# Optimization experiments

Measured on AMD Instinct MI355X. Metric: run time of the kernel, lower is better.

Reference implementation:

```python
import jax, jax.numpy as jnp
import numpy as np

N = 50000
E = 500000
IN_F = 128
HEADS = 4
NEG_SLOPE = 0.2


def _gatv2_conv(x, src, dst, Wl, Wr, att, bias, concat):
    # PyG GATv2Conv (share_weights=False): x_l = lin_l(x) for source, x_r = lin_r(x) for target
    n = x.shape[0]
    H, C = att.shape
    xl = (x @ Wl.T).reshape(n, H, C)
    xr = (x @ Wr.T).reshape(n, H, C)
    # per-edge: e_ij = att . leaky_relu(xl[j] + xr[i])
    e = jax.nn.leaky_relu(xl[src] + xr[dst], negative_slope=NEG_SLOPE)  # [E,H,C]
    logit = jnp.einsum('ehc,hc->eh', e, att)  # [E,H]
    # segment softmax over destination node
    lmax = jax.ops.segment_max(logit, dst, num_segments=n)
    lmax = jnp.where(jnp.isfinite(lmax), lmax, 0.0)
    w = jnp.exp(logit - lmax[dst])
    denom = jax.ops.segment_sum(w, dst, num_segments=n)
    alpha = w / (denom[dst] + 1e-16)
    # weighted scatter-aggregate of source messages
    out = jax.ops.segment_sum(xl[src] * alpha[:, :, None], dst, num_segments=n)  # [N,H,C]
    if concat:
        return out.reshape(n, H * C) + bias
    return out.mean(axis=1) + bias


def setup_inputs() -> dict:
    key = jax.random.key(0)
    ks = jax.random.split(key, 11)
    s = 0.1
    x = jax.random.normal(ks[0], (N, IN_F), jnp.float32)
    edge_index = jax.random.randint(ks[1], (2, E), 0, N, dtype=jnp.int32)
    # layer 1: in=128 -> heads=4, C=32, concat -> out 128
    Wl1 = jax.random.normal(ks[2], (128, IN_F), jnp.float32) * s
    Wr1 = jax.random.normal(ks[3], (128, IN_F), jnp.float32) * s
    att1 = jax.random.normal(ks[4], (HEADS, 32), jnp.float32) * s
    b1 = jnp.zeros((128,), jnp.float32)
    # layer 2: in=128 -> heads=4, C=64, mean (concat=False) -> out 64
    Wl2 = jax.random.normal(ks[5], (256, 128), jnp.float32) * s
    Wr2 = jax.random.normal(ks[6], (256, 128), jnp.float32) * s
    att2 = jax.random.normal(ks[7], (HEADS, 64), jnp.float32) * s
    b2 = jnp.zeros((64,), jnp.float32)
    return {"x": x, "edge_index": edge_index, "Wl1": Wl1, "Wr1": Wr1, "att1": att1,
            "b1": b1, "Wl2": Wl2, "Wr2": Wr2, "att2": att2, "b2": b2}


def reference(x, edge_index, Wl1, Wr1, att1, b1, Wl2, Wr2, att2, b2):
    n = x.shape[0]
    loops = jnp.arange(n, dtype=edge_index.dtype)
    src = jnp.concatenate([edge_index[0], loops])  # PyG add_self_loops=True
    dst = jnp.concatenate([edge_index[1], loops])
    # dropout inactive (inference); forward body: elu between layers
    h = jax.nn.elu(_gatv2_conv(x, src, dst, Wl1, Wr1, att1, b1, concat=True))
    logits = _gatv2_conv(h, src, dst, Wl2, Wr2, att2, b2, concat=False)
    return logits
```

## Files before the change

### kernel.cpp

```cpp
#include <hip/hip_runtime.h>
#include <hip/hip_bf16.h>
#include <math.h>


typedef _Float16 half2v __attribute__((ext_vector_type(2)));
typedef _Float16 half4v __attribute__((ext_vector_type(4)));
typedef _Float16 half8v __attribute__((ext_vector_type(8)));
typedef float float4v __attribute__((ext_vector_type(4)));

template <int CTRL>
static __device__ __forceinline__ float dppadd(float x) {
  int y = __builtin_amdgcn_update_dpp(0, __float_as_int(x), CTRL, 0xf, 0xf, true);
  return x + __int_as_float(y);
}

static __device__ __forceinline__ float red16dpp(float p) {
  p = dppadd<0xB1>(p);
  p = dppadd<0x4E>(p);
  p = dppadd<0x140>(p);
  p = dppadd<0x141>(p);
  return p;
}


__global__ void cvt_all_kernel(const float* __restrict__ x,
                               const float* __restrict__ wl1, const float* __restrict__ wr1,
                               const float* __restrict__ wl2, const float* __restrict__ wr2,
                               _Float16* __restrict__ xb, _Float16* __restrict__ wb, int n4x) {
  int i = blockIdx.x * blockDim.x + threadIdx.x;
  int stride = gridDim.x * blockDim.x;
  int total = n4x + 24576;
  for (; i < total; i += stride) {
    if (i < n4x) {
      float4 v = ((const float4*)x)[i];
      half4v o = {(_Float16)v.x, (_Float16)v.y, (_Float16)v.z, (_Float16)v.w};
      ((half4v*)xb)[i] = o;
    } else {
      int fj = (i - n4x) * 4;
      const float* src;
      int so;
      if (fj < 16384) { src = wl1; so = fj; }
      else if (fj < 32768) { src = wr1; so = fj - 16384; }
      else if (fj < 65536) { src = wl2; so = fj - 32768; }
      else { src = wr2; so = fj - 65536; }
      float4 v = *(const float4*)(src + so);
      half4v o = {(_Float16)v.x, (_Float16)v.y, (_Float16)v.z, (_Float16)v.w};
      *(half4v*)(wb + fj) = o;
    }
  }
}


__global__ void count_kernel(const int* __restrict__ dst, int* __restrict__ deg, int E) {
  int i = blockIdx.x * blockDim.x + threadIdx.x;
  if (i < E) atomicAdd(&deg[dst[i]], 1);
}

__global__ void partial_kernel(const int* __restrict__ deg, int* __restrict__ partial, int N) {
  int t = threadIdx.x;
  int i = blockIdx.x * 256 + t;
  int v = (i < N) ? deg[i] : 0;
  v += __shfl_xor(v, 1); v += __shfl_xor(v, 2); v += __shfl_xor(v, 4);
  v += __shfl_xor(v, 8); v += __shfl_xor(v, 16); v += __shfl_xor(v, 32);
  __shared__ int ws[4];
  if ((t & 63) == 0) ws[t >> 6] = v;
  __syncthreads();
  if (t == 0) partial[blockIdx.x] = ws[0] + ws[1] + ws[2] + ws[3];
}

__global__ void scan_partials_kernel(int* __restrict__ partial, int nb) {
  __shared__ int s[256];
  int t = threadIdx.x;
  int v = (t < nb) ? partial[t] : 0;
  s[t] = v;
  __syncthreads();
  for (int off = 1; off < 256; off <<= 1) {
    int u = (t >= off) ? s[t - off] : 0;
    __syncthreads();
    s[t] += u;
    __syncthreads();
  }
  if (t < nb) partial[t] = s[t] - v;
}

__global__ void scan_final_kernel(const int* __restrict__ deg, const int* __restrict__ partial,
                                  int* __restrict__ row_ptr, int* __restrict__ cursor,
                                  int N, int E) {
  __shared__ int s[256];
  int t = threadIdx.x;
  int i = blockIdx.x * 256 + t;
  int v = (i < N) ? deg[i] : 0;
  s[t] = v;
  __syncthreads();
  for (int off = 1; off < 256; off <<= 1) {
    int u = (t >= off) ? s[t - off] : 0;
    __syncthreads();
    s[t] += u;
    __syncthreads();
  }
  int excl = s[t] - v + partial[blockIdx.x];
  if (i < N) {
    row_ptr[i] = excl;
    cursor[i] = excl;
  }
  if (blockIdx.x == 0 && t == 0) row_ptr[N] = E;
}

__global__ void fill_kernel(const int* __restrict__ src, const int* __restrict__ dst,
                            int* __restrict__ cursor, int* __restrict__ col, int E) {
  int i = blockIdx.x * blockDim.x + threadIdx.x;
  if (i < E) {
    int d = dst[i];
    int pos = atomicAdd(&cursor[d], 1);
    col[pos] = src[i];
  }
}

__global__ __launch_bounds__(256) void gemm_mfma2(
    const _Float16* __restrict__ A, const _Float16* __restrict__ Wa,
    const _Float16* __restrict__ Wb, _Float16* __restrict__ Ca,
    _Float16* __restrict__ Cb, int N, int Oa, int ldC) {
  __shared__ _Float16 lds[32768];
  int t = threadIdx.x;
  int gbase = blockIdx.y * 256;
#pragma unroll
  for (int i = 0; i < 16; ++i) {
    int c = t + i * 256;
    int row = c >> 4, kc = c & 15;
    int grow = gbase + row;
    const _Float16* srcW =
        (grow < Oa) ? (Wa + (size_t)grow * 128) : (Wb + (size_t)(grow - Oa) * 128);
    half8v v = *(const half8v*)(srcW + kc * 8);
    int off16 = (row << 4) | (kc ^ (row & 7));
    *(half8v*)((char*)lds + (off16 << 4)) = v;
  }
  __syncthreads();
  int wv = t >> 6, lane = t & 63;
  int l15 = lane & 15, l4 = lane >> 4;
  int row0 = blockIdx.x * 64 + (wv & 1) * 32;
  int colw = (wv >> 1) * 128;
  int gc = gbase + colw;
  half8v xf[2][4];
#pragma unroll
  for (int rg = 0; rg < 2; ++rg) {
    int r = row0 + rg * 16 + l15;
    bool valid = r < N;
    const half8v* Ar = (const half8v*)(A + (size_t)r * 128 + l4 * 8);
#pragma unroll
    for (int kk = 0; kk < 4; ++kk) {
      half8v z = {};
      xf[rg][kk] = valid ? Ar[kk * 4] : z;
    }
  }
  int wrow = colw + l15;
  float4v acc[2][8] = {};
#pragma unroll
  for (int kk = 0; kk < 4; ++kk) {
    int xorterm = ((kk * 4 + l4) ^ (l15 & 7)) << 4;
    const char* base = (const char*)lds + wrow * 256 + xorterm;
    half8v wf[8];
#pragma unroll
    for (int ot = 0; ot < 8; ++ot) wf[ot] = *(const half8v*)(base + ot * 4096);
#pragma unroll
    for (int ot = 0; ot < 8; ++ot) {
      acc[0][ot] = __builtin_amdgcn_mfma_f32_16x16x32_f16(wf[ot], xf[0][kk], acc[0][ot], 0, 0, 0);
      acc[1][ot] = __builtin_amdgcn_mfma_f32_16x16x32_f16(wf[ot], xf[1][kk], acc[1][ot], 0, 0, 0);
    }
  }
  bool isA = gc < Oa;
  _Float16* C = isA ? Ca : Cb;
  int cb = isA ? gc : gc - Oa;
#pragma unroll
  for (int rg = 0; rg < 2; ++rg) {
    int r = row0 + rg * 16 + l15;
    if (r < N) {
#pragma unroll
      for (int ot = 0; ot < 8; ++ot) {
        half4v o = {(_Float16)acc[rg][ot][0], (_Float16)acc[rg][ot][1],
                    (_Float16)acc[rg][ot][2], (_Float16)acc[rg][ot][3]};
        *(half4v*)(C + (size_t)r * ldC + cb + ot * 16 + l4 * 4) = o;
      }
    }
  }
}


__global__ __launch_bounds__(256) void agg1_kernel(
    const _Float16* __restrict__ xl, const _Float16* __restrict__ xr,
    const float* __restrict__ att, const float* __restrict__ bias,
    const int* __restrict__ row_ptr, const int* __restrict__ col,
    _Float16* __restrict__ hout, int N) {
  int wid = (blockIdx.x * blockDim.x + threadIdx.x) >> 6;
  int lane = threadIdx.x & 63;
  if (wid >= N) return;
  const int d0 = lane * 2;
  half2v xrv = *(const half2v*)(xr + (size_t)wid * 128 + d0);
  float2 atf = *(const float2*)(att + d0);
  half2v at = {(_Float16)atf.x, (_Float16)atf.y};
  half2v k2 = {(_Float16)0.2f, (_Float16)0.2f};
  float2 bi = *(const float2*)(bias + d0);
  int e0 = row_ptr[wid], eend = row_ptr[wid + 1];
  int total = eend - e0 + 1;
  int i1 = (total > 1) ? col[e0] : 0;
  half2v vA = *(const half2v*)(xl + (size_t)wid * 128 + d0);
  half2v vB = *(const half2v*)(xl + (size_t)i1 * 128 + d0);
  float s = 0.f, a0 = 0.f, a1 = 0.f;
  for (int j = 0; j < total; ++j) {
    int nIdx = (j + 2 < total) ? col[e0 + j + 1] : 0;
    half2v vC = *(const half2v*)(xl + (size_t)nIdx * 128 + d0);
    half2v u = vA + xrv;
    half2v lr = __builtin_elementwise_max(u, u * k2);
    float p = __builtin_amdgcn_fdot2(lr, at, 0.f, false);
    p = red16dpp(p);
    float w = __expf(p);
    s += w;
    a0 = fmaf(w, (float)vA.x, a0);
    a1 = fmaf(w, (float)vA.y, a1);
    vA = vB;
    vB = vC;
  }
  float inv = 1.f / (s + 1e-16f);
  float ox = a0 * inv + bi.x;
  float oy = a1 * inv + bi.y;
  ox = ox > 0.f ? ox : __expf(ox) - 1.f;
  oy = oy > 0.f ? oy : __expf(oy) - 1.f;
  half2v o = {(_Float16)ox, (_Float16)oy};
  *(half2v*)(hout + (size_t)wid * 128 + d0) = o;
}

__global__ __launch_bounds__(256) void agg2_kernel(
    const _Float16* __restrict__ xl, const _Float16* __restrict__ xr,
    const float* __restrict__ att, const float* __restrict__ bias,
    const int* __restrict__ row_ptr, const int* __restrict__ col,
    float* __restrict__ out, int N) {
  int wid = (blockIdx.x * blockDim.x + threadIdx.x) >> 6;
  int lane = threadIdx.x & 63;
  if (wid >= N) return;
  const int d0 = lane * 4;
  half4v xrv = *(const half4v*)(xr + (size_t)wid * 256 + d0);
  float4 atf = *(const float4*)(att + d0);
  half2v atlo = {(_Float16)atf.x, (_Float16)atf.y};
  half2v athi = {(_Float16)atf.z, (_Float16)atf.w};
  half4v k4 = {(_Float16)0.2f, (_Float16)0.2f, (_Float16)0.2f, (_Float16)0.2f};
  int e0 = row_ptr[wid], eend = row_ptr[wid + 1];
  int total = eend - e0 + 1;
  int i1 = (total > 1) ? col[e0] : 0;
  half4v vA = *(const half4v*)(xl + (size_t)wid * 256 + d0);
  half4v vB = *(const half4v*)(xl + (size_t)i1 * 256 + d0);
  float s = 0.f, a0 = 0.f, a1 = 0.f, a2 = 0.f, a3 = 0.f;
  for (int j = 0; j < total; ++j) {
    int nIdx = (j + 2 < total) ? col[e0 + j + 1] : 0;
    half4v vC = *(const half4v*)(xl + (size_t)nIdx * 256 + d0);
    half4v u = vA + xrv;
    half4v lr = __builtin_elementwise_max(u, u * k4);
    half2v lo = __builtin_shufflevector(lr, lr, 0, 1);
    half2v hi = __builtin_shufflevector(lr, lr, 2, 3);
    float p = __builtin_amdgcn_fdot2(lo, atlo, 0.f, false);
    p = __builtin_amdgcn_fdot2(hi, athi, p, false);
    p = red16dpp(p);
    float w = __expf(p);
    s += w;
    a0 = fmaf(w, (float)vA.x, a0);
    a1 = fmaf(w, (float)vA.y, a1);
    a2 = fmaf(w, (float)vA.z, a2);
    a3 = fmaf(w, (float)vA.w, a3);
    vA = vB;
    vB = vC;
  }
  float inv = 1.f / (s + 1e-16f);
  float vx = a0 * inv, vy = a1 * inv, vz = a2 * inv, vw = a3 * inv;
  vx += __shfl_xor(vx, 16); vx += __shfl_xor(vx, 32);
  vy += __shfl_xor(vy, 16); vy += __shfl_xor(vy, 32);
  vz += __shfl_xor(vz, 16); vz += __shfl_xor(vz, 32);
  vw += __shfl_xor(vw, 16); vw += __shfl_xor(vw, 32);
  if (lane < 16) {
    float4 b = *(const float4*)(bias + d0);
    float4 o = make_float4(vx * 0.25f + b.x, vy * 0.25f + b.y,
                           vz * 0.25f + b.z, vw * 0.25f + b.w);
    *(float4*)(out + (size_t)wid * 64 + d0) = o;
  }
}

extern "C" void kernel_launch(void* const* d_in, const int* in_sizes, int n_in,
                              void* d_out, int out_size, void* d_ws, size_t ws_size,
                              hipStream_t stream) {
  const float* x = (const float*)d_in[0];
  const int* ei = (const int*)d_in[1];
  const float* Wl1 = (const float*)d_in[2];
  const float* Wr1 = (const float*)d_in[3];
  const float* att1 = (const float*)d_in[4];
  const float* b1 = (const float*)d_in[5];
  const float* Wl2 = (const float*)d_in[6];
  const float* Wr2 = (const float*)d_in[7];
  const float* att2 = (const float*)d_in[8];
  const float* b2 = (const float*)d_in[9];
  float* out = (float*)d_out;

  int N = in_sizes[0] / 128;
  int E = in_sizes[1] / 2;
  const int* srcArr = ei;
  const int* dstArr = ei + E;

  char* w = (char*)d_ws;
  auto alloc = [&](size_t bytes) {
    char* p = w;
    w += (bytes + 255) & ~(size_t)255;
    return p;
  };
  int* row_ptr = (int*)alloc((size_t)(N + 1) * sizeof(int));
  int* cursor = (int*)alloc((size_t)N * sizeof(int));
  int* partial = (int*)alloc(256 * sizeof(int));
  int* col = (int*)alloc((size_t)E * sizeof(int));
  _Float16* xb = (_Float16*)alloc((size_t)N * 128 * 2);
  _Float16* wb = (_Float16*)alloc(98304 * 2);
  _Float16* hb = (_Float16*)alloc((size_t)N * 128 * 2);
  _Float16* xl1 = (_Float16*)alloc((size_t)N * 128 * 2);
  _Float16* xr1 = (_Float16*)alloc((size_t)N * 128 * 2);
  _Float16* xl2 = (_Float16*)alloc((size_t)N * 256 * 2);
  _Float16* xr2 = (_Float16*)alloc((size_t)N * 256 * 2);

  const _Float16* wl1b = wb;
  const _Float16* wr1b = wb + 16384;
  const _Float16* wl2b = wb + 32768;
  const _Float16* wr2b = wb + 65536;

  cvt_all_kernel<<<1024, 256, 0, stream>>>(x, Wl1, Wr1, Wl2, Wr2, xb, wb, N * 32);

  hipMemsetAsync(cursor, 0, (size_t)N * sizeof(int), stream);
  count_kernel<<<(E + 255) / 256, 256, 0, stream>>>(dstArr, cursor, E);
  int nb = (N + 255) / 256;
  partial_kernel<<<nb, 256, 0, stream>>>(cursor, partial, N);
  scan_partials_kernel<<<1, 256, 0, stream>>>(partial, nb);
  scan_final_kernel<<<nb, 256, 0, stream>>>(cursor, partial, row_ptr, cursor, N, E);
  fill_kernel<<<(E + 255) / 256, 256, 0, stream>>>(srcArr, dstArr, cursor, col, E);

  int gx = (N + 63) / 64;
  gemm_mfma2<<<dim3(gx, 1), 256, 0, stream>>>(xb, wl1b, wr1b, xl1, xr1, N, 128, 128);
  agg1_kernel<<<(N * 64 + 255) / 256, 256, 0, stream>>>(xl1, xr1, att1, b1, row_ptr, col, hb, N);

  gemm_mfma2<<<dim3(gx, 2), 256, 0, stream>>>(hb, wl2b, wr2b, xl2, xr2, N, 256, 256);
  agg2_kernel<<<(N * 64 + 255) / 256, 256, 0, stream>>>(xl2, xr2, att2, b2, row_ptr, col, out, N);
}
```

Baseline: 213.1 us.

## Split each wave into two half-waves processing alternate edges in aggregation

Both aggregation kernels now split a 64-lane wave into two 32-lane halves. Each half handles every other edge of the destination node, with wider per-lane vectors (4 halves for layer 1, 8 for layer 2). Per-head reductions shrink to 8 lanes, and the two halves' partial softmax sums and accumulators are combined with a cross-half shuffle at the end. The goal is to halve the serial edge-loop length per node and issue wider loads, in exchange for extra shuffles and some masked-off work when the degree is odd.

```diff
diff --git a/kernel.cpp b/kernel.cpp
--- a/kernel.cpp
+++ b/kernel.cpp
@@ -14,10 +14,9 @@
   return x + __int_as_float(y);
 }
 
-static __device__ __forceinline__ float red16dpp(float p) {
+static __device__ __forceinline__ float red8dpp(float p) {
   p = dppadd<0xB1>(p);
   p = dppadd<0x4E>(p);
-  p = dppadd<0x140>(p);
   p = dppadd<0x141>(p);
   return p;
 }
@@ -193,39 +192,68 @@
   int wid = (blockIdx.x * blockDim.x + threadIdx.x) >> 6;
   int lane = threadIdx.x & 63;
   if (wid >= N) return;
-  const int d0 = lane * 2;
-  half2v xrv = *(const half2v*)(xr + (size_t)wid * 128 + d0);
-  float2 atf = *(const float2*)(att + d0);
-  half2v at = {(_Float16)atf.x, (_Float16)atf.y};
-  half2v k2 = {(_Float16)0.2f, (_Float16)0.2f};
-  float2 bi = *(const float2*)(bias + d0);
-  int e0 = row_ptr[wid], eend = row_ptr[wid + 1];
-  int total = eend - e0 + 1;
-  int i1 = (total > 1) ? col[e0] : 0;
-  half2v vA = *(const half2v*)(xl + (size_t)wid * 128 + d0);
-  half2v vB = *(const half2v*)(xl + (size_t)i1 * 128 + d0);
-  float s = 0.f, a0 = 0.f, a1 = 0.f;
-  for (int j = 0; j < total; ++j) {
-    int nIdx = (j + 2 < total) ? col[e0 + j + 1] : 0;
-    half2v vC = *(const half2v*)(xl + (size_t)nIdx * 128 + d0);
-    half2v u = vA + xrv;
-    half2v lr = __builtin_elementwise_max(u, u * k2);
-    float p = __builtin_amdgcn_fdot2(lr, at, 0.f, false);
-    p = red16dpp(p);
-    float w = __expf(p);
-    s += w;
-    a0 = fmaf(w, (float)vA.x, a0);
-    a1 = fmaf(w, (float)vA.y, a1);
-    vA = vB;
-    vB = vC;
-  }
+  int eslot = lane >> 5, sub = lane & 31;
+  const int d0 = sub * 4;
+  const _Float16* xld = xl + d0;
+  half4v xrv = *(const half4v*)(xr + (size_t)wid * 128 + d0);
+  float4 atf = *(const float4*)(att + d0);
+  half2v atlo = {(_Float16)atf.x, (_Float16)atf.y};
+  half2v athi = {(_Float16)atf.z, (_Float16)atf.w};
+  half4v k4 = {(_Float16)0.2f, (_Float16)0.2f, (_Float16)0.2f, (_Float16)0.2f};
+  int e0 = row_ptr[wid];
+  int deg = row_ptr[wid + 1] - e0;
+  float s, a0, a1, a2, a3;
+  {
+    half4v v = *(const half4v*)(xld + (size_t)wid * 128);
+    half4v u = v + xrv;
+    half4v lr = __builtin_elementwise_max(u, u * k4);
+    float p = __builtin_amdgcn_fdot2((half2v){lr.x, lr.y}, atlo, 0.f, false);
+    p = __builtin_amdgcn_fdot2((half2v){lr.z, lr.w}, athi, p, false);
+    p = red8dpp(p);
+    float w = (eslot == 0) ? __expf(p) : 0.f;
+    s = w;
+    a0 = w * (float)v.x; a1 = w * (float)v.y; a2 = w * (float)v.z; a3 = w * (float)v.w;
+  }
+  int niter = (deg + 1) >> 1;
+  if (niter > 0) {
+    int idx = eslot;
+    bool valid = idx < deg;
+    int srcn = col[e0 + (valid ? idx : 0)];
+    half4v vcur = *(const half4v*)(xld + (size_t)srcn * 128);
+    for (int j = 0; j < niter; ++j) {
+      int nidx = idx + 2;
+      bool nvalid = nidx < deg;
+      int nsrc = col[e0 + (nvalid ? nidx : 0)];
+      half4v vnxt = *(const half4v*)(xld + (size_t)nsrc * 128);
+      half4v u = vcur + xrv;
+      half4v lr = __builtin_elementwise_max(u, u * k4);
+      float p = __builtin_amdgcn_fdot2((half2v){lr.x, lr.y}, atlo, 0.f, false);
+      p = __builtin_amdgcn_fdot2((half2v){lr.z, lr.w}, athi, p, false);
+      p = red8dpp(p);
+      float w = valid ? __expf(p) : 0.f;
+      s += w;
+      a0 = fmaf(w, (float)vcur.x, a0);
+      a1 = fmaf(w, (float)vcur.y, a1);
+      a2 = fmaf(w, (float)vcur.z, a2);
+      a3 = fmaf(w, (float)vcur.w, a3);
+      vcur = vnxt; idx = nidx; valid = nvalid;
+    }
+  }
+  s += __shfl_xor(s, 32);
+  a0 += __shfl_xor(a0, 32); a1 += __shfl_xor(a1, 32);
+  a2 += __shfl_xor(a2, 32); a3 += __shfl_xor(a3, 32);
   float inv = 1.f / (s + 1e-16f);
-  float ox = a0 * inv + bi.x;
-  float oy = a1 * inv + bi.y;
-  ox = ox > 0.f ? ox : __expf(ox) - 1.f;
-  oy = oy > 0.f ? oy : __expf(oy) - 1.f;
-  half2v o = {(_Float16)ox, (_Float16)oy};
-  *(half2v*)(hout + (size_t)wid * 128 + d0) = o;
+  float4 bi = *(const float4*)(bias + d0);
+  float o0 = a0 * inv + bi.x, o1 = a1 * inv + bi.y;
+  float o2 = a2 * inv + bi.z, o3 = a3 * inv + bi.w;
+  o0 = o0 > 0.f ? o0 : __expf(o0) - 1.f;
+  o1 = o1 > 0.f ? o1 : __expf(o1) - 1.f;
+  o2 = o2 > 0.f ? o2 : __expf(o2) - 1.f;
+  o3 = o3 > 0.f ? o3 : __expf(o3) - 1.f;
+  if (eslot == 0) {
+    half4v o = {(_Float16)o0, (_Float16)o1, (_Float16)o2, (_Float16)o3};
+    *(half4v*)(hout + (size_t)wid * 128 + d0) = o;
+  }
 }
 
 __global__ __launch_bounds__(256) void agg2_kernel(
@@ -236,48 +264,79 @@
   int wid = (blockIdx.x * blockDim.x + threadIdx.x) >> 6;
   int lane = threadIdx.x & 63;
   if (wid >= N) return;
-  const int d0 = lane * 4;
-  half4v xrv = *(const half4v*)(xr + (size_t)wid * 256 + d0);
-  float4 atf = *(const float4*)(att + d0);
-  half2v atlo = {(_Float16)atf.x, (_Float16)atf.y};
-  half2v athi = {(_Float16)atf.z, (_Float16)atf.w};
-  half4v k4 = {(_Float16)0.2f, (_Float16)0.2f, (_Float16)0.2f, (_Float16)0.2f};
-  int e0 = row_ptr[wid], eend = row_ptr[wid + 1];
-  int total = eend - e0 + 1;
-  int i1 = (total > 1) ? col[e0] : 0;
-  half4v vA = *(const half4v*)(xl + (size_t)wid * 256 + d0);
-  half4v vB = *(const half4v*)(xl + (size_t)i1 * 256 + d0);
-  float s = 0.f, a0 = 0.f, a1 = 0.f, a2 = 0.f, a3 = 0.f;
-  for (int j = 0; j < total; ++j) {
-    int nIdx = (j + 2 < total) ? col[e0 + j + 1] : 0;
-    half4v vC = *(const half4v*)(xl + (size_t)nIdx * 256 + d0);
-    half4v u = vA + xrv;
-    half4v lr = __builtin_elementwise_max(u, u * k4);
-    half2v lo = __builtin_shufflevector(lr, lr, 0, 1);
-    half2v hi = __builtin_shufflevector(lr, lr, 2, 3);
-    float p = __builtin_amdgcn_fdot2(lo, atlo, 0.f, false);
-    p = __builtin_amdgcn_fdot2(hi, athi, p, false);
-    p = red16dpp(p);
-    float w = __expf(p);
-    s += w;
-    a0 = fmaf(w, (float)vA.x, a0);
-    a1 = fmaf(w, (float)vA.y, a1);
-    a2 = fmaf(w, (float)vA.z, a2);
-    a3 = fmaf(w, (float)vA.w, a3);
-    vA = vB;
-    vB = vC;
-  }
+  int eslot = lane >> 5, sub = lane & 31;
+  const int d0 = sub * 8;
+  const _Float16* xld = xl + d0;
+  half8v xrv = *(const half8v*)(xr + (size_t)wid * 256 + d0);
+  float4 af0 = *(const float4*)(att + d0);
+  float4 af1 = *(const float4*)(att + d0 + 4);
+  half2v at[4] = {{(_Float16)af0.x, (_Float16)af0.y}, {(_Float16)af0.z, (_Float16)af0.w},
+                  {(_Float16)af1.x, (_Float16)af1.y}, {(_Float16)af1.z, (_Float16)af1.w}};
+  half8v k8 = {(_Float16)0.2f, (_Float16)0.2f, (_Float16)0.2f, (_Float16)0.2f,
+               (_Float16)0.2f, (_Float16)0.2f, (_Float16)0.2f, (_Float16)0.2f};
+  int e0 = row_ptr[wid];
+  int deg = row_ptr[wid + 1] - e0;
+  float s, ac[8];
+  {
+    half8v v = *(const half8v*)(xld + (size_t)wid * 256);
+    half8v u = v + xrv;
+    half8v lr = __builtin_elementwise_max(u, u * k8);
+    float p = __builtin_amdgcn_fdot2((half2v){lr[0], lr[1]}, at[0], 0.f, false);
+    p = __builtin_amdgcn_fdot2((half2v){lr[2], lr[3]}, at[1], p, false);
+    p = __builtin_amdgcn_fdot2((half2v){lr[4], lr[5]}, at[2], p, false);
+    p = __builtin_amdgcn_fdot2((half2v){lr[6], lr[7]}, at[3], p, false);
+    p = red8dpp(p);
+    float w = (eslot == 0) ? __expf(p) : 0.f;
+    s = w;
+#pragma unroll
+    for (int k = 0; k < 8; ++k) ac[k] = w * (float)v[k];
+  }
+  int niter = (deg + 1) >> 1;
+  if (niter > 0) {
+    int idx = eslot;
+    bool valid = idx < deg;
+    int srcn = col[e0 + (valid ? idx : 0)];
+    half8v vcur = *(const half8v*)(xld + (size_t)srcn * 256);
+    for (int j = 0; j < niter; ++j) {
+      int nidx = idx + 2;
+      bool nvalid = nidx < deg;
+      int nsrc = col[e0 + (nvalid ? nidx : 0)];
+      half8v vnxt = *(const half8v*)(xld + (size_t)nsrc * 256);
+      half8v u = vcur + xrv;
+      half8v lr = __builtin_elementwise_max(u, u * k8);
+      float p = __builtin_amdgcn_fdot2((half2v){lr[0], lr[1]}, at[0], 0.f, false);
+      p = __builtin_amdgcn_fdot2((half2v){lr[2], lr[3]}, at[1], p, false);
+      p = __builtin_amdgcn_fdot2((half2v){lr[4], lr[5]}, at[2], p, false);
+      p = __builtin_amdgcn_fdot2((half2v){lr[6], lr[7]}, at[3], p, false);
+      p = red8dpp(p);
+      float w = valid ? __expf(p) : 0.f;
+      s += w;
+#pragma unroll
+      for (int k = 0; k < 8; ++k) ac[k] = fmaf(w, (float)vcur[k], ac[k]);
+      vcur = vnxt; idx = nidx; valid = nvalid;
+    }
+  }
+  s += __shfl_xor(s, 32);
+#pragma unroll
+  for (int k = 0; k < 8; ++k) ac[k] += __shfl_xor(ac[k], 32);
   float inv = 1.f / (s + 1e-16f);
-  float vx = a0 * inv, vy = a1 * inv, vz = a2 * inv, vw = a3 * inv;
-  vx += __shfl_xor(vx, 16); vx += __shfl_xor(vx, 32);
-  vy += __shfl_xor(vy, 16); vy += __shfl_xor(vy, 32);
-  vz += __shfl_xor(vz, 16); vz += __shfl_xor(vz, 32);
-  vw += __shfl_xor(vw, 16); vw += __shfl_xor(vw, 32);
-  if (lane < 16) {
-    float4 b = *(const float4*)(bias + d0);
-    float4 o = make_float4(vx * 0.25f + b.x, vy * 0.25f + b.y,
-                           vz * 0.25f + b.z, vw * 0.25f + b.w);
-    *(float4*)(out + (size_t)wid * 64 + d0) = o;
+#pragma unroll
+  for (int k = 0; k < 8; ++k) ac[k] *= inv;
+#pragma unroll
+  for (int k = 0; k < 8; ++k) {
+    ac[k] += __shfl_xor(ac[k], 8);
+    ac[k] += __shfl_xor(ac[k], 16);
+  }
+  if (lane < 8) {
+    float4 b0 = *(const float4*)(bias + lane * 8);
+    float4 b1v = *(const float4*)(bias + lane * 8 + 4);
+    float4 o0 = make_float4(ac[0] * 0.25f + b0.x, ac[1] * 0.25f + b0.y,
+                            ac[2] * 0.25f + b0.z, ac[3] * 0.25f + b0.w);
+    float4 o1 = make_float4(ac[4] * 0.25f + b1v.x, ac[5] * 0.25f + b1v.y,
+                            ac[6] * 0.25f + b1v.z, ac[7] * 0.25f + b1v.w);
+    float* op = out + (size_t)wid * 64 + lane * 8;
+    *(float4*)op = o0;
+    *(float4*)(op + 4) = o1;
   }
 }
 
```

Result: faster. 202.7 us (-4.9%).
